# Kernel optimization log

Hardware: AMD Instinct MI355X
Metric: run time of the kernel (lower is better)

Reference implementation:

```python
import jax, jax.numpy as jnp
import numpy as np

GRID_ROWS, GRID_COLS = 7, 10
GRID_SIZE = GRID_ROWS * GRID_COLS  # 70
CONTEXT_SIZE = 24
STATE_SIZE = GRID_SIZE + CONTEXT_SIZE  # 94
H = 128  # LSTM_HIDDEN


def setup_inputs() -> dict:
    key = jax.random.key(0)
    ks = jax.random.split(key, 16)
    B, T = 1024, 128
    inp = {
        'states_seq': jax.random.normal(ks[0], (B, T, STATE_SIZE), jnp.float32),
        'actions_seq': jax.random.randint(ks[1], (B, T), 0, 4).astype(jnp.int32),
        # conv params (OIHW)
        'conv1_w': jax.random.normal(ks[2], (16, 1, 3, 3), jnp.float32) * 0.3,
        'conv1_b': jnp.zeros((16,), jnp.float32),
        'conv2_w': jax.random.normal(ks[3], (32, 16, 3, 3), jnp.float32) * 0.08,
        'conv2_b': jnp.zeros((32,), jnp.float32),
        # dense params (out, in) like torch Linear
        'grid_fc_w': jax.random.normal(ks[4], (128, 32 * GRID_SIZE), jnp.float32) * 0.02,
        'grid_fc_b': jnp.zeros((128,), jnp.float32),
        'ctx_fc_w': jax.random.normal(ks[5], (64, CONTEXT_SIZE), jnp.float32) * 0.2,
        'ctx_fc_b': jnp.zeros((64,), jnp.float32),
        'trunk_w': jax.random.normal(ks[6], (128, 192), jnp.float32) * 0.07,
        'trunk_b': jnp.zeros((128,), jnp.float32),
        # LSTM params
        'W_ih': jax.random.normal(ks[7], (4 * H, 128), jnp.float32) * 0.09,
        'b_ih': jnp.zeros((4 * H,), jnp.float32),
        'W_hh': jax.random.normal(ks[8], (4 * H, H), jnp.float32) * 0.09,
        # heads
        'actor_w': jax.random.uniform(ks[9], (4, H), jnp.float32, -0.01, 0.01),
        'actor_b': jnp.zeros((4,), jnp.float32),
        'critic_w': jax.random.uniform(ks[10], (1, H), jnp.float32, -0.01, 0.01),
        'critic_b': jnp.zeros((1,), jnp.float32),
    }
    return inp


def _forward(states_seq, actions_seq, conv1_w, conv1_b, conv2_w, conv2_b,
             grid_fc_w, grid_fc_b, ctx_fc_w, ctx_fc_b, trunk_w, trunk_b,
             W_ih, b_ih, W_hh, actor_w, actor_b, critic_w, critic_b):
    B, T, _ = states_seq.shape
    x = states_seq.reshape(-1, STATE_SIZE)                  # (N, 94)
    grid = x[:, :GRID_SIZE].reshape(-1, 1, GRID_ROWS, GRID_COLS)
    ctx = x[:, GRID_SIZE:]
    g = jax.lax.conv_general_dilated(grid, conv1_w, (1, 1), 'SAME',
                                     dimension_numbers=('NCHW', 'OIHW', 'NCHW'))
    g = jax.nn.relu(g + conv1_b[None, :, None, None])
    g = jax.lax.conv_general_dilated(g, conv2_w, (1, 1), 'SAME',
                                     dimension_numbers=('NCHW', 'OIHW', 'NCHW'))
    g = jax.nn.relu(g + conv2_b[None, :, None, None])
    g = g.reshape(g.shape[0], -1)                           # (N, 2240)
    g = jax.nn.relu(g @ grid_fc_w.T + grid_fc_b)            # (N, 128)
    c = jax.nn.relu(ctx @ ctx_fc_w.T + ctx_fc_b)            # (N, 64)
    trunk = jax.nn.relu(jnp.concatenate([g, c], -1) @ trunk_w.T + trunk_b)
    trunk = trunk.reshape(B, T, 128)

    # LSTM: precompute input-to-gate GEMM for all timesteps, scan over time
    gates_x = jnp.einsum('btd,gd->tbg', trunk, W_ih) + b_ih  # (T, B, 4H)

    def step(carry, gx):
        h, cst = carry
        gates = gx + h @ W_hh.T
        i, f, gg, o = jnp.split(gates, 4, axis=-1)
        i, f, o = jax.nn.sigmoid(i), jax.nn.sigmoid(f), jax.nn.sigmoid(o)
        gg = jnp.tanh(gg)
        cst = f * cst + i * gg
        h = o * jnp.tanh(cst)
        return (h, cst), h

    h0 = jnp.zeros((B, H), trunk.dtype)
    _, hs = jax.lax.scan(step, (h0, h0), gates_x)            # hs: (T, B, H)
    h_flat = jnp.transpose(hs, (1, 0, 2)).reshape(B * T, H)

    logits = h_flat @ actor_w.T + actor_b                    # (N, 4)
    values = (h_flat @ critic_w.T + critic_b)[:, 0]          # (N,)
    logp = jax.nn.log_softmax(logits, axis=-1)
    a = actions_seq.reshape(-1)
    log_probs = jnp.take_along_axis(logp, a[:, None].astype(jnp.int32), axis=-1)[:, 0]
    entropy = -jnp.sum(jnp.exp(logp) * logp, axis=-1)
    return log_probs, values, entropy


def reference(states_seq, actions_seq, conv1_w, conv1_b, conv2_w, conv2_b,
              grid_fc_w, grid_fc_b, ctx_fc_w, ctx_fc_b, trunk_w, trunk_b,
              W_ih, b_ih, W_hh, actor_w, actor_b, critic_w, critic_b):
    return _forward(states_seq, actions_seq, conv1_w, conv1_b, conv2_w, conv2_b,
                    grid_fc_w, grid_fc_b, ctx_fc_w, ctx_fc_b, trunk_w, trunk_b,
                    W_ih, b_ih, W_hh, actor_w, actor_b, critic_w, critic_b)
```

## Files before the change

### kernel.cpp

```cpp
#include <hip/hip_runtime.h>
#include <hip/hip_bf16.h>

typedef unsigned int  u32;
typedef unsigned short u16;
typedef unsigned long long u64;
typedef __attribute__((ext_vector_type(8))) short bf16x8;
typedef __attribute__((ext_vector_type(4))) float f32x4;

#define B_   1024
#define T_   128
#define NBT  (B_*T_)
#define CHUNK 32768
#define NCHUNK 4

#define WG_OFF   0
#define WT_OFF   286720
#define WIH_OFF  311296
#define W2_OFF   376832
#define W1C_OFF  381952
#define CVT_TOTAL 382464

#define TRUNK_OFF (1ull<<20)
#define H_OFF     (36ull<<20)
#define CTX_OFF   (72ull<<20)
#define C2_OFF    (92ull<<20)

__device__ __forceinline__ u16 f2bf(float f){
  __hip_bfloat16 h = __float2bfloat16(f);
  return *reinterpret_cast<u16*>(&h);
}
__device__ __forceinline__ float bf2f(u16 u){ return __uint_as_float((u32)u << 16); }
__device__ __forceinline__ float sigm(float x){ return 1.f / (1.f + __expf(-x)); }
__device__ __forceinline__ float tanh_f(float x){ return 2.f / (1.f + __expf(-2.f*x)) - 1.f; }

__device__ __forceinline__ void bar_lds() {
  __builtin_amdgcn_sched_barrier(0);
  asm volatile("s_waitcnt lgkmcnt(0)" ::: "memory");
  __builtin_amdgcn_s_barrier();
  __builtin_amdgcn_sched_barrier(0);
}

__global__ void k_cvt(const float* __restrict__ gfw, const float* __restrict__ tw,
                      const float* __restrict__ wih, const float* __restrict__ c2w,
                      const float* __restrict__ c1w, u16* __restrict__ wsb) {
  int i = blockIdx.x * 256 + threadIdx.x;
  if (i >= CVT_TOTAL) return;
  float v;
  if (i < WT_OFF) {
    int o = i / 2240; int k = i - o*2240;
    int pos = k >> 5, ch = k & 31;
    v = gfw[o*2240 + ch*70 + pos];
  }
  else if (i < WIH_OFF)  v = tw[i - WT_OFF];
  else if (i < W2_OFF)   v = wih[i - WIH_OFF];
  else if (i < W1C_OFF) {
    int j = i - W2_OFF; int co = j / 160; int k = j - co*160;
    int tap = k >> 4; int ci = k & 15;
    v = (tap < 9) ? c2w[co*144 + ci*9 + tap] : 0.f;
  } else {
    int j = i - W1C_OFF; int ch = j >> 5; int k = j & 31;
    v = (k < 9) ? c1w[ch*9 + k] : 0.f;
  }
  wsb[i] = f2bf(v);
}

__global__ __launch_bounds__(512, 4) void k_conv(
    const float* __restrict__ states,
    const float* __restrict__ c1b, const float* __restrict__ c2b,
    const float* __restrict__ cfw, const float* __restrict__ cfb,
    const u16* __restrict__ wsb,
    u16* __restrict__ c2g,
    u16* __restrict__ ctxg)
{
  __shared__ float s_st[8][96];
  __shared__ __align__(16) u16 act1[8*108*16];

  const int tid  = threadIdx.x;
  const int lane = tid & 63;
  const int w    = tid >> 6;
  const int arow = lane & 15;
  const int grp  = lane >> 4;
  const int g0   = blockIdx.x * 64;

  bf16x8 Bc1 = *(const bf16x8*)(wsb + W1C_OFF + arow*32 + grp*8);
  bf16x8 b2f[5][2];
  #pragma unroll
  for (int p = 0; p < 5; p++)
    #pragma unroll
    for (int nt = 0; nt < 2; nt++)
      b2f[p][nt] = *(const bf16x8*)(wsb + W2_OFF + (nt*16 + arow)*160 + p*32 + grp*8);
  float c1bv[4], c2bv0[4], c2bv1[4];
  #pragma unroll
  for (int r = 0; r < 4; r++) {
    c1bv[r]  = c1b[grp*4 + r];
    c2bv0[r] = c2b[grp*4 + r];
    c2bv1[r] = c2b[16 + grp*4 + r];
  }
  const float cfbr = cfb[lane];
  float cfwr[24];
  #pragma unroll
  for (int k = 0; k < 24; k++) cfwr[k] = cfw[lane*24 + k];

  const int sst_s = (tid*2)/94, sst_c = (tid*2)%94;

  if (tid < 376) {
    float2 v = *(const float2*)(states + (size_t)g0*94 + tid*2);
    *(float2*)&s_st[sst_s][sst_c] = v;
  }
  for (int i = tid; i < 608; i += 512) {
    int s = i / 76; int r = i - s*76; int hi2 = r >> 1; int h = r & 1;
    int hp;
    if (hi2 < 12)      hp = hi2;
    else if (hi2 < 24) hp = 96 + (hi2 - 12);
    else if (hi2 < 31) hp = (hi2 - 23) * 12;
    else               hp = (hi2 - 30) * 12 + 11;
    u32 a = (u32)((s*108 + hp)*32 + h*16) ^ (u32)((hp & 7) << 4);
    *(uint4*)((char*)act1 + a) = (uint4){0,0,0,0};
  }
  bar_lds();

  const bf16x8 zv = {0,0,0,0,0,0,0,0};

  for (int g = 0; g < 8; g++) {
    const int m0 = g0 + g*8;
    float2 npre;
    const bool haspre = (g < 7) && (tid < 376);
    if (haspre)
      npre = *(const float2*)(states + (size_t)(m0 + 8)*94 + tid*2);

    for (int mt = w; mt < 35; mt += 8) {
      int row = mt*16 + arow;
      int s = (int)(((u32)row * 59919u) >> 22); int pos = row - s*70;
      int y = (int)(((u32)pos * 6554u) >> 16);  int x = pos - y*10;
      bf16x8 pf = zv;
      if (grp == 0) {
        const float* gs = &s_st[s][0];
        #pragma unroll
        for (int t = 0; t < 8; t++) {
          int dy = t/3, dx = t - (t/3)*3;
          int yy = y + dy - 1, xx = x + dx - 1;
          bool ok = (yy >= 0) & (yy < 7) & (xx >= 0) & (xx < 10);
          float v = gs[ok ? yy*10 + xx : 0];
          pf[t] = (short)f2bf(ok ? v : 0.f);
        }
      } else if (grp == 1) {
        int yy = y + 1, xx = x + 1;
        bool ok = (yy < 7) & (xx < 10);
        float v = s_st[s][ok ? yy*10 + xx : 0];
        pf[0] = (short)f2bf(ok ? v : 0.f);
      }
      f32x4 acc = __builtin_amdgcn_mfma_f32_16x16x32_bf16(Bc1, pf, (f32x4){0.f,0.f,0.f,0.f}, 0, 0, 0);
      int hp = (y+1)*12 + (x+1);
      u16 q0 = f2bf(fmaxf(acc[0] + c1bv[0], 0.f));
      u16 q1 = f2bf(fmaxf(acc[1] + c1bv[1], 0.f));
      u16 q2 = f2bf(fmaxf(acc[2] + c1bv[2], 0.f));
      u16 q3 = f2bf(fmaxf(acc[3] + c1bv[3], 0.f));
      u64 pk = (u64)q0 | ((u64)q1 << 16) | ((u64)q2 << 32) | ((u64)q3 << 48);
      u32 wa = (u32)(((s*108 + hp)*16 + grp*4)*2) ^ (u32)((hp & 7) << 4);
      *(u64*)((char*)act1 + wa) = pk;
    }
    bar_lds();

    for (int mt = w; mt < 35; mt += 8) {
      int row = mt*16 + arow;
      int s = (int)(((u32)row * 59919u) >> 22); int pos = row - s*70;
      int y = (int)(((u32)pos * 6554u) >> 16);  int x = pos - y*10;
      f32x4 acc0 = {0.f,0.f,0.f,0.f}, acc1 = {0.f,0.f,0.f,0.f};
      #pragma unroll
      for (int p = 0; p < 5; p++) {
        int tap = p*2 + (grp >> 1); if (tap > 8) tap = 8;
        int dy = (tap * 11) >> 5; int dx = tap - dy*3;
        int hp = (y + dy)*12 + (x + dx);
        u32 ra = (u32)(((s*108 + hp)*16 + (grp & 1)*8)*2) ^ (u32)((hp & 7) << 4);
        bf16x8 bv = *(const bf16x8*)((const char*)act1 + ra);
        acc0 = __builtin_amdgcn_mfma_f32_16x16x32_bf16(b2f[p][0], bv, acc0, 0, 0, 0);
        acc1 = __builtin_amdgcn_mfma_f32_16x16x32_bf16(b2f[p][1], bv, acc1, 0, 0, 0);
      }
      {
        u16 q0 = f2bf(fmaxf(acc0[0] + c2bv0[0], 0.f));
        u16 q1 = f2bf(fmaxf(acc0[1] + c2bv0[1], 0.f));
        u16 q2 = f2bf(fmaxf(acc0[2] + c2bv0[2], 0.f));
        u16 q3 = f2bf(fmaxf(acc0[3] + c2bv0[3], 0.f));
        u64 pk = (u64)q0 | ((u64)q1 << 16) | ((u64)q2 << 32) | ((u64)q3 << 48);
        *(u64*)(c2g + (size_t)(m0 + s)*2240 + pos*32 + grp*4) = pk;
      }
      {
        u16 q0 = f2bf(fmaxf(acc1[0] + c2bv1[0], 0.f));
        u16 q1 = f2bf(fmaxf(acc1[1] + c2bv1[1], 0.f));
        u16 q2 = f2bf(fmaxf(acc1[2] + c2bv1[2], 0.f));
        u16 q3 = f2bf(fmaxf(acc1[3] + c2bv1[3], 0.f));
        u64 pk = (u64)q0 | ((u64)q1 << 16) | ((u64)q2 << 32) | ((u64)q3 << 48);
        *(u64*)(c2g + (size_t)(m0 + s)*2240 + pos*32 + 16 + grp*4) = pk;
      }
    }
    {
      float a = cfbr;
      #pragma unroll
      for (int k = 0; k < 24; k++) a = fmaf(cfwr[k], s_st[w][70 + k], a);
      ctxg[(size_t)(m0 + w)*64 + lane] = f2bf(fmaxf(a, 0.f));
    }

    if (g < 7) {
      bar_lds();
      if (haspre) *(float2*)&s_st[sst_s][sst_c] = npre;
      bar_lds();
    }
  }
}

__global__ __launch_bounds__(512, 2) void k_gemm(
    const u16* __restrict__ c2g, const u16* __restrict__ ctxg,
    const float* __restrict__ gfb, const float* __restrict__ tbv,
    const u16* __restrict__ wsb, u16* __restrict__ trunk_ws, int nbase)
{
  __shared__ __align__(16) u16 s_b[2][128*72];
  __shared__ __align__(16) u16 s_g[64*204];

  const int tid  = threadIdx.x;
  const int lane = tid & 63;
  const int w    = tid >> 6;
  const int arow = lane & 15;
  const int grp  = lane >> 4;
  const int wm   = w & 3;
  const int wn   = w >> 2;
  const int m0   = blockIdx.x * 64;

  float gfbv[4], tbvv[4];
  #pragma unroll
  for (int q = 0; q < 4; q++) {
    gfbv[q] = gfb[(wn*4 + q)*16 + arow];
    tbvv[q] = tbv[(wn*4 + q)*16 + arow];
  }

  const int srow = tid >> 2, sseg = (tid & 3) * 16;
  const u16* wg = wsb + WG_OFF;
  const u16* ap = c2g + (size_t)(m0 + wm*16 + arow) * 2240 + grp*8;

  {
    const u16* src = wg + (size_t)srow*2240 + sseg;
    *(uint4*)&s_b[0][srow*72 + sseg]     = *(const uint4*)src;
    *(uint4*)&s_b[0][srow*72 + sseg + 8] = *(const uint4*)(src + 8);
  }
  bf16x8 aC0 = *(const bf16x8*)(ap);
  bf16x8 aC1 = *(const bf16x8*)(ap + 32);
  bf16x8 aN0 = *(const bf16x8*)(ap + 64);
  bf16x8 aN1 = *(const bf16x8*)(ap + 96);
  f32x4 acc[4];
  #pragma unroll
  for (int q = 0; q < 4; q++) acc[q] = (f32x4){0.f,0.f,0.f,0.f};
  __syncthreads();

  for (int kp = 0; kp < 35; kp++) {
    uint4 b0v, b1v;
    if (kp < 34) {
      const u16* src = wg + (size_t)srow*2240 + (kp+1)*64 + sseg;
      b0v = *(const uint4*)src;
      b1v = *(const uint4*)(src + 8);
    }
    bf16x8 aF0 = aN0, aF1 = aN1;
    if (kp < 33) {
      aF0 = *(const bf16x8*)(ap + (size_t)(kp+2)*64);
      aF1 = *(const bf16x8*)(ap + (size_t)(kp+2)*64 + 32);
    }
    const u16* sb = &s_b[kp & 1][0];
    #pragma unroll
    for (int q = 0; q < 4; q++) {
      bf16x8 bv0 = *(const bf16x8*)&sb[((wn*4 + q)*16 + arow)*72 + grp*8];
      acc[q] = __builtin_amdgcn_mfma_f32_16x16x32_bf16(aC0, bv0, acc[q], 0, 0, 0);
    }
    #pragma unroll
    for (int q = 0; q < 4; q++) {
      bf16x8 bv1 = *(const bf16x8*)&sb[((wn*4 + q)*16 + arow)*72 + 32 + grp*8];
      acc[q] = __builtin_amdgcn_mfma_f32_16x16x32_bf16(aC1, bv1, acc[q], 0, 0, 0);
    }
    if (kp < 34) {
      *(uint4*)&s_b[(kp+1) & 1][srow*72 + sseg]     = b0v;
      *(uint4*)&s_b[(kp+1) & 1][srow*72 + sseg + 8] = b1v;
    }
    aC0 = aN0; aC1 = aN1; aN0 = aF0; aN1 = aF1;
    bar_lds();
  }

  #pragma unroll
  for (int q = 0; q < 4; q++)
    #pragma unroll
    for (int r = 0; r < 4; r++)
      s_g[(wm*16 + grp*4 + r)*204 + (wn*4 + q)*16 + arow] = f2bf(fmaxf(acc[q][r] + gfbv[q], 0.f));
  {
    int row = tid >> 3, seg = (tid & 7) * 8;
    uint4 c0 = *(const uint4*)(ctxg + (size_t)(m0 + row)*64 + seg);
    *(uint4*)&s_g[row*204 + 128 + seg] = c0;
  }
  bar_lds();

  f32x4 tacc[4];
  #pragma unroll
  for (int q = 0; q < 4; q++) tacc[q] = (f32x4){0.f,0.f,0.f,0.f};
  #pragma unroll
  for (int ks = 0; ks < 6; ks++) {
    bf16x8 av = *(const bf16x8*)&s_g[(wm*16 + arow)*204 + ks*32 + grp*8];
    #pragma unroll
    for (int q = 0; q < 4; q++) {
      bf16x8 bv = *(const bf16x8*)(wsb + WT_OFF + (size_t)((wn*4 + q)*16 + arow)*192 + ks*32 + grp*8);
      tacc[q] = __builtin_amdgcn_mfma_f32_16x16x32_bf16(av, bv, tacc[q], 0, 0, 0);
    }
  }
  bar_lds();
  #pragma unroll
  for (int q = 0; q < 4; q++)
    #pragma unroll
    for (int r = 0; r < 4; r++)
      s_g[(wm*16 + grp*4 + r)*204 + (wn*4 + q)*16 + arow] = f2bf(fmaxf(tacc[q][r] + tbvv[q], 0.f));
  bar_lds();

  {
    const int t0 = (nbase + m0) & 127;
    const int bb = (nbase + m0) >> 7;
    int row = tid >> 3, seg = (tid & 7) * 16;
    #pragma unroll
    for (int j = 0; j < 2; j++) {
      uint4 v = *(const uint4*)&s_g[row*204 + seg + j*8];
      *(uint4*)(trunk_ws + ((size_t)(t0 + row)*B_ + bb)*128 + seg + j*8) = v;
    }
  }
}

__global__ __launch_bounds__(512, 1) void k_lstm(
    const u16* __restrict__ trunk_ws, const float* __restrict__ whh,
    const float* __restrict__ wih, const float* __restrict__ bih,
    u16* __restrict__ h_ws)
{
  __shared__ __align__(16) u16 s_h[2][16*136];
  __shared__ __align__(16) u16 s_tk[3][4*136];

  const int tid  = threadIdx.x;
  const int lane = tid & 63;
  const int w    = tid >> 6;
  const int arow = lane & 15;
  const int grp  = lane >> 4;
  const int b0   = blockIdx.x * 4;

  bf16x8 Bv[4][4], Bw[4][4];
  float bihv[4];
  #pragma unroll
  for (int j = 0; j < 4; j++) {
    const int row = j*128 + w*16 + arow;
    bihv[j] = bih[row];
    #pragma unroll
    for (int ks = 0; ks < 4; ks++) {
      const float* s1 = whh + (size_t)row*128 + ks*32 + grp*8;
      const float* s2 = wih + (size_t)row*128 + ks*32 + grp*8;
      float4 a0 = *(const float4*)s1, a1 = *(const float4*)(s1 + 4);
      float4 b0v = *(const float4*)s2, b1v = *(const float4*)(s2 + 4);
      bf16x8 t1, t2;
      t1[0]=(short)f2bf(a0.x); t1[1]=(short)f2bf(a0.y); t1[2]=(short)f2bf(a0.z); t1[3]=(short)f2bf(a0.w);
      t1[4]=(short)f2bf(a1.x); t1[5]=(short)f2bf(a1.y); t1[6]=(short)f2bf(a1.z); t1[7]=(short)f2bf(a1.w);
      t2[0]=(short)f2bf(b0v.x); t2[1]=(short)f2bf(b0v.y); t2[2]=(short)f2bf(b0v.z); t2[3]=(short)f2bf(b0v.w);
      t2[4]=(short)f2bf(b1v.x); t2[5]=(short)f2bf(b1v.y); t2[6]=(short)f2bf(b1v.z); t2[7]=(short)f2bf(b1v.w);
      Bv[j][ks] = t1; Bw[j][ks] = t2;
    }
  }

  for (int i = tid; i < 2*16*136; i += 512) ((u16*)s_h)[i] = 0;

  const int prow = tid >> 4, pseg = (tid & 15) * 8;
  if (tid < 64) {
    #pragma unroll
    for (int s = 0; s < 3; s++)
      *(uint4*)&s_tk[s][prow*136 + pseg] =
          *(const uint4*)(trunk_ws + ((size_t)s*B_ + b0 + prow)*128 + pseg);
  }
  uint4 P0 = {0,0,0,0};
  if (tid < 64)
    P0 = *(const uint4*)(trunk_ws + ((size_t)3*B_ + b0 + prow)*128 + pseg);

  float cst = 0.f;
  __syncthreads();

  f32x4 xA[4];
  #pragma unroll
  for (int j = 0; j < 4; j++) xA[j] = (f32x4){0.f,0.f,0.f,0.f};
  #pragma unroll
  for (int ks = 0; ks < 4; ks++) {
    bf16x8 av = *(const bf16x8*)&s_tk[0][(arow & 3)*136 + ks*32 + grp*8];
    #pragma unroll
    for (int j = 0; j < 4; j++)
      xA[j] = __builtin_amdgcn_mfma_f32_16x16x32_bf16(av, Bw[j][ks], xA[j], 0, 0, 0);
  }

  for (int t = 0; t < T_; t++) {
    const int p = t & 1;

    uint4 P1 = {0,0,0,0};
    if ((t + 4 < T_) && tid < 64)
      P1 = *(const uint4*)(trunk_ws + ((size_t)(t+4)*B_ + b0 + prow)*128 + pseg);

    if (t > 0 && tid < 64) {
      uint4 hv = *(const uint4*)&s_h[p][prow*136 + pseg];
      *(uint4*)(h_ws + ((size_t)(t-1)*B_ + b0 + prow)*128 + pseg) = hv;
    }

    f32x4 racc[4], xB[4];
    #pragma unroll
    for (int j = 0; j < 4; j++) { racc[j] = (f32x4){0.f,0.f,0.f,0.f}; xB[j] = (f32x4){0.f,0.f,0.f,0.f}; }
    #pragma unroll
    for (int ks = 0; ks < 4; ks++) {
      bf16x8 av = *(const bf16x8*)&s_h[p][arow*136 + ks*32 + grp*8];
      #pragma unroll
      for (int j = 0; j < 4; j++)
        racc[j] = __builtin_amdgcn_mfma_f32_16x16x32_bf16(av, Bv[j][ks], racc[j], 0, 0, 0);
    }
    {
      const u16* tk = &s_tk[(t+1) % 3][0];
      #pragma unroll
      for (int ks = 0; ks < 4; ks++) {
        bf16x8 av = *(const bf16x8*)&tk[(arow & 3)*136 + ks*32 + grp*8];
        #pragma unroll
        for (int j = 0; j < 4; j++)
          xB[j] = __builtin_amdgcn_mfma_f32_16x16x32_bf16(av, Bw[j][ks], xB[j], 0, 0, 0);
      }
    }

    float g4[4];
    #pragma unroll
    for (int j = 0; j < 4; j++) {
      float s0 = racc[j][0] + xA[j][0];
      float s1 = racc[j][1] + xA[j][1];
      float s2 = racc[j][2] + xA[j][2];
      float s3 = racc[j][3] + xA[j][3];
      float t0v = __shfl(s0, arow);
      float t1v = __shfl(s1, arow);
      float t2v = __shfl(s2, arow);
      float t3v = __shfl(s3, arow);
      g4[j] = (grp == 0) ? t0v : (grp == 1) ? t1v : (grp == 2) ? t2v : t3v;
    }

    {
      float xi = g4[0] + bihv[0];
      float xf = g4[1] + bihv[1];
      float xg = g4[2] + bihv[2];
      float xo = g4[3] + bihv[3];
      float I = sigm(xi), F = sigm(xf), O = sigm(xo), G = tanh_f(xg);
      cst = F*cst + I*G;
      float hvv = O * tanh_f(cst);
      s_h[1-p][grp*136 + w*16 + arow] = f2bf(hvv);
    }

    if ((t + 3 < T_) && tid < 64)
      *(uint4*)&s_tk[t % 3][prow*136 + pseg] = P0;
    P0 = P1;
    #pragma unroll
    for (int j = 0; j < 4; j++) xA[j] = xB[j];
    bar_lds();
  }

  if (tid < 64) {
    uint4 hv = *(const uint4*)&s_h[T_ & 1][prow*136 + pseg];
    *(uint4*)(h_ws + ((size_t)(T_-1)*B_ + b0 + prow)*128 + pseg) = hv;
  }
}

__global__ __launch_bounds__(256, 1) void k_heads(
    const u16* __restrict__ h_ws, const int* __restrict__ actions,
    const float* __restrict__ aw, const float* __restrict__ ab,
    const float* __restrict__ cw, const float* __restrict__ cb,
    float* __restrict__ out)
{
  const int tid  = threadIdx.x;
  const int lane = tid & 63;
  const int w    = tid >> 6;
  const int arow = lane & 15;
  const int grp  = lane >> 4;

  bf16x8 Ah[4];
  #pragma unroll
  for (int ks = 0; ks < 4; ks++) {
    bf16x8 v = {0,0,0,0,0,0,0,0};
    if (arow < 4) {
      const float* src = aw + arow*128 + ks*32 + grp*8;
      #pragma unroll
      for (int j = 0; j < 8; j++) v[j] = (short)f2bf(src[j]);
    } else if (arow == 4) {
      const float* src = cw + ks*32 + grp*8;
      #pragma unroll
      for (int j = 0; j < 8; j++) v[j] = (short)f2bf(src[j]);
    }
    Ah[ks] = v;
  }
  const float ab0=ab[0], ab1=ab[1], ab2=ab[2], ab3=ab[3], cb0=cb[0];

  #pragma unroll
  for (int g = 0; g < 4; g++) {
    int m0 = (blockIdx.x*4 + w)*64 + g*16;
    int t  = m0 >> 10; int bb = m0 & 1023;
    f32x4 acc = {0.f,0.f,0.f,0.f};
    #pragma unroll
    for (int ks = 0; ks < 4; ks++) {
      bf16x8 bv = *(const bf16x8*)(h_ws + ((size_t)t*B_ + bb + arow)*128 + ks*32 + grp*8);
      acc = __builtin_amdgcn_mfma_f32_16x16x32_bf16(Ah[ks], bv, acc, 0, 0, 0);
    }
    float cr = __shfl_xor(acc[0], 16);
    if (grp == 0) {
      float L0 = acc[0] + ab0, L1 = acc[1] + ab1, L2 = acc[2] + ab2, L3 = acc[3] + ab3;
      float Lv = cr + cb0;
      float mm = fmaxf(fmaxf(L0, L1), fmaxf(L2, L3));
      float e0 = __expf(L0-mm), e1 = __expf(L1-mm), e2 = __expf(L2-mm), e3 = __expf(L3-mm);
      float S = e0+e1+e2+e3; float lse = __logf(S);
      float p0=L0-mm-lse, p1=L1-mm-lse, p2=L2-mm-lse, p3=L3-mm-lse;
      int n = (bb + arow)*T_ + t;
      int a = actions[n];
      float lpa = (a==0)?p0:(a==1)?p1:(a==2)?p2:p3;
      float ent = -(e0*p0 + e1*p1 + e2*p2 + e3*p3) / S;
      out[n] = lpa; out[NBT + n] = Lv; out[2*NBT + n] = ent;
    }
  }
}

extern "C" void kernel_launch(void* const* d_in, const int* in_sizes, int n_in,
                              void* d_out, int out_size, void* d_ws, size_t ws_size,
                              hipStream_t stream) {
  const float* states = (const float*)d_in[0];
  const int*   actions= (const int*)  d_in[1];
  const float* c1w = (const float*)d_in[2];
  const float* c1b = (const float*)d_in[3];
  const float* c2w = (const float*)d_in[4];
  const float* c2b = (const float*)d_in[5];
  const float* gfw = (const float*)d_in[6];
  const float* gfb = (const float*)d_in[7];
  const float* cfw = (const float*)d_in[8];
  const float* cfb = (const float*)d_in[9];
  const float* tw  = (const float*)d_in[10];
  const float* tbv = (const float*)d_in[11];
  const float* wih = (const float*)d_in[12];
  const float* bih = (const float*)d_in[13];
  const float* whh = (const float*)d_in[14];
  const float* aw  = (const float*)d_in[15];
  const float* ab  = (const float*)d_in[16];
  const float* cw  = (const float*)d_in[17];
  const float* cb  = (const float*)d_in[18];
  float* out = (float*)d_out;

  u16* wsb   = (u16*)d_ws;
  u16* trunk = (u16*)((char*)d_ws + TRUNK_OFF);
  u16* h_ws  = (u16*)((char*)d_ws + H_OFF);
  u16* ctxg  = (u16*)((char*)d_ws + CTX_OFF);
  u16* c2g   = (u16*)((char*)d_ws + C2_OFF);

  k_cvt<<<(CVT_TOTAL + 255)/256, 256, 0, stream>>>(gfw, tw, wih, c2w, c1w, wsb);

  for (int c = 0; c < NCHUNK; c++) {
    const float* st_c = states + (size_t)c * CHUNK * 94;
    u16* ctx_c = ctxg + (size_t)c * CHUNK * 64;
    k_conv<<<CHUNK/64, 512, 0, stream>>>(st_c, c1b, c2b, cfw, cfb, wsb, c2g, ctx_c);
    k_gemm<<<CHUNK/64, 512, 0, stream>>>(c2g, ctx_c, gfb, tbv, wsb, trunk, c*CHUNK);
  }
  k_lstm<<<B_/4, 512, 0, stream>>>(trunk, whh, wih, bih, h_ws);
  k_heads<<<512, 256, 0, stream>>>(h_ws, actions, aw, ab, cw, cb, out);
}
```

Baseline: 690.3 us.

## Software-pipeline conv and gemm stages in a fused kernel with double buffers

Replaces the alternating conv and gemm launches per chunk with one fused kernel per step. Each launch runs the conv of chunk i in some blocks and the gemm of chunk i-1 in the others, using two ping-pong intermediate buffers and a smaller chunk size. The aim is to overlap the compute-heavy conv with the gemm and cut per-launch tail idle time. In exchange the fused kernel uses a shared LDS footprint sized for the larger stage with launch bounds of 2, which lowers conv occupancy, and there are more launches.

```diff
diff --git a/kernel.cpp b/kernel.cpp
--- a/kernel.cpp
+++ b/kernel.cpp
@@ -10,8 +10,8 @@
 #define B_   1024
 #define T_   128
 #define NBT  (B_*T_)
-#define CHUNK 32768
-#define NCHUNK 4
+#define CH   16384
+#define NCH  8
 
 #define WG_OFF   0
 #define WT_OFF   286720
@@ -23,7 +23,8 @@
 #define TRUNK_OFF (1ull<<20)
 #define H_OFF     (36ull<<20)
 #define CTX_OFF   (72ull<<20)
-#define C2_OFF    (92ull<<20)
+#define C2A_OFF   (92ull<<20)
+#define C2B_OFF   (C2A_OFF + 74ull*1024*1024)
 
 __device__ __forceinline__ u16 f2bf(float f){
   __hip_bfloat16 h = __float2bfloat16(f);
@@ -64,23 +65,22 @@
   wsb[i] = f2bf(v);
 }
 
-__global__ __launch_bounds__(512, 4) void k_conv(
-    const float* __restrict__ states,
+__device__ void conv_body(char* smem,
+    const float* __restrict__ states_c,
     const float* __restrict__ c1b, const float* __restrict__ c2b,
     const float* __restrict__ cfw, const float* __restrict__ cfb,
     const u16* __restrict__ wsb,
-    u16* __restrict__ c2g,
-    u16* __restrict__ ctxg)
+    u16* __restrict__ c2buf, u16* __restrict__ ctx_c, int blk)
 {
-  __shared__ float s_st[8][96];
-  __shared__ __align__(16) u16 act1[8*108*16];
+  float (*s_st)[96] = (float(*)[96])smem;
+  u16* act1 = (u16*)(smem + 3072);
 
   const int tid  = threadIdx.x;
   const int lane = tid & 63;
   const int w    = tid >> 6;
   const int arow = lane & 15;
   const int grp  = lane >> 4;
-  const int g0   = blockIdx.x * 64;
+  const int g0   = blk * 64;
 
   bf16x8 Bc1 = *(const bf16x8*)(wsb + W1C_OFF + arow*32 + grp*8);
   bf16x8 b2f[5][2];
@@ -104,7 +104,7 @@
   const int sst_s = (tid*2)/94, sst_c = (tid*2)%94;
 
   if (tid < 376) {
-    float2 v = *(const float2*)(states + (size_t)g0*94 + tid*2);
+    float2 v = *(const float2*)(states_c + (size_t)g0*94 + tid*2);
     *(float2*)&s_st[sst_s][sst_c] = v;
   }
   for (int i = tid; i < 608; i += 512) {
@@ -115,7 +115,7 @@
     else if (hi2 < 31) hp = (hi2 - 23) * 12;
     else               hp = (hi2 - 30) * 12 + 11;
     u32 a = (u32)((s*108 + hp)*32 + h*16) ^ (u32)((hp & 7) << 4);
-    *(uint4*)((char*)act1 + a) = (uint4){0,0,0,0};
+    *(uint4*)(act1 ? (char*)act1 + a : 0) = (uint4){0,0,0,0};
   }
   bar_lds();
 
@@ -126,7 +126,7 @@
     float2 npre;
     const bool haspre = (g < 7) && (tid < 376);
     if (haspre)
-      npre = *(const float2*)(states + (size_t)(m0 + 8)*94 + tid*2);
+      npre = *(const float2*)(states_c + (size_t)(m0 + 8)*94 + tid*2);
 
     for (int mt = w; mt < 35; mt += 8) {
       int row = mt*16 + arow;
@@ -182,7 +182,7 @@
         u16 q2 = f2bf(fmaxf(acc0[2] + c2bv0[2], 0.f));
         u16 q3 = f2bf(fmaxf(acc0[3] + c2bv0[3], 0.f));
         u64 pk = (u64)q0 | ((u64)q1 << 16) | ((u64)q2 << 32) | ((u64)q3 << 48);
-        *(u64*)(c2g + (size_t)(m0 + s)*2240 + pos*32 + grp*4) = pk;
+        *(u64*)(c2buf + (size_t)(m0 + s)*2240 + pos*32 + grp*4) = pk;
       }
       {
         u16 q0 = f2bf(fmaxf(acc1[0] + c2bv1[0], 0.f));
@@ -190,14 +190,14 @@
         u16 q2 = f2bf(fmaxf(acc1[2] + c2bv1[2], 0.f));
         u16 q3 = f2bf(fmaxf(acc1[3] + c2bv1[3], 0.f));
         u64 pk = (u64)q0 | ((u64)q1 << 16) | ((u64)q2 << 32) | ((u64)q3 << 48);
-        *(u64*)(c2g + (size_t)(m0 + s)*2240 + pos*32 + 16 + grp*4) = pk;
+        *(u64*)(c2buf + (size_t)(m0 + s)*2240 + pos*32 + 16 + grp*4) = pk;
       }
     }
     {
       float a = cfbr;
       #pragma unroll
       for (int k = 0; k < 24; k++) a = fmaf(cfwr[k], s_st[w][70 + k], a);
-      ctxg[(size_t)(m0 + w)*64 + lane] = f2bf(fmaxf(a, 0.f));
+      ctx_c[(size_t)(m0 + w)*64 + lane] = f2bf(fmaxf(a, 0.f));
     }
 
     if (g < 7) {
@@ -208,13 +208,14 @@
   }
 }
 
-__global__ __launch_bounds__(512, 2) void k_gemm(
-    const u16* __restrict__ c2g, const u16* __restrict__ ctxg,
+__device__ void gemm_body(char* smem,
+    const u16* __restrict__ c2buf, const u16* __restrict__ ctx_c,
     const float* __restrict__ gfb, const float* __restrict__ tbv,
-    const u16* __restrict__ wsb, u16* __restrict__ trunk_ws, int nbase)
+    const u16* __restrict__ wsb, u16* __restrict__ trunk_ws,
+    int nbase, int blk)
 {
-  __shared__ __align__(16) u16 s_b[2][128*72];
-  __shared__ __align__(16) u16 s_g[64*204];
+  u16* s_b = (u16*)smem;
+  u16* s_g = (u16*)(smem + 36864);
 
   const int tid  = threadIdx.x;
   const int lane = tid & 63;
@@ -223,7 +224,7 @@
   const int grp  = lane >> 4;
   const int wm   = w & 3;
   const int wn   = w >> 2;
-  const int m0   = blockIdx.x * 64;
+  const int m0   = blk * 64;
 
   float gfbv[4], tbvv[4];
   #pragma unroll
@@ -234,12 +235,12 @@
 
   const int srow = tid >> 2, sseg = (tid & 3) * 16;
   const u16* wg = wsb + WG_OFF;
-  const u16* ap = c2g + (size_t)(m0 + wm*16 + arow) * 2240 + grp*8;
+  const u16* ap = c2buf + (size_t)(m0 + wm*16 + arow) * 2240 + grp*8;
 
   {
     const u16* src = wg + (size_t)srow*2240 + sseg;
-    *(uint4*)&s_b[0][srow*72 + sseg]     = *(const uint4*)src;
-    *(uint4*)&s_b[0][srow*72 + sseg + 8] = *(const uint4*)(src + 8);
+    *(uint4*)&s_b[srow*72 + sseg]     = *(const uint4*)src;
+    *(uint4*)&s_b[srow*72 + sseg + 8] = *(const uint4*)(src + 8);
   }
   bf16x8 aC0 = *(const bf16x8*)(ap);
   bf16x8 aC1 = *(const bf16x8*)(ap + 32);
@@ -262,7 +263,7 @@
       aF0 = *(const bf16x8*)(ap + (size_t)(kp+2)*64);
       aF1 = *(const bf16x8*)(ap + (size_t)(kp+2)*64 + 32);
     }
-    const u16* sb = &s_b[kp & 1][0];
+    const u16* sb = &s_b[(kp & 1)*9216];
     #pragma unroll
     for (int q = 0; q < 4; q++) {
       bf16x8 bv0 = *(const bf16x8*)&sb[((wn*4 + q)*16 + arow)*72 + grp*8];
@@ -274,8 +275,8 @@
       acc[q] = __builtin_amdgcn_mfma_f32_16x16x32_bf16(aC1, bv1, acc[q], 0, 0, 0);
     }
     if (kp < 34) {
-      *(uint4*)&s_b[(kp+1) & 1][srow*72 + sseg]     = b0v;
-      *(uint4*)&s_b[(kp+1) & 1][srow*72 + sseg + 8] = b1v;
+      *(uint4*)&s_b[((kp+1) & 1)*9216 + srow*72 + sseg]     = b0v;
+      *(uint4*)&s_b[((kp+1) & 1)*9216 + srow*72 + sseg + 8] = b1v;
     }
     aC0 = aN0; aC1 = aN1; aN0 = aF0; aN1 = aF1;
     bar_lds();
@@ -288,7 +289,7 @@
       s_g[(wm*16 + grp*4 + r)*204 + (wn*4 + q)*16 + arow] = f2bf(fmaxf(acc[q][r] + gfbv[q], 0.f));
   {
     int row = tid >> 3, seg = (tid & 7) * 8;
-    uint4 c0 = *(const uint4*)(ctxg + (size_t)(m0 + row)*64 + seg);
+    uint4 c0 = *(const uint4*)(ctx_c + (size_t)(m0 + row)*64 + seg);
     *(uint4*)&s_g[row*204 + 128 + seg] = c0;
   }
   bar_lds();
@@ -322,6 +323,30 @@
       uint4 v = *(const uint4*)&s_g[row*204 + seg + j*8];
       *(uint4*)(trunk_ws + ((size_t)(t0 + row)*B_ + bb)*128 + seg + j*8) = v;
     }
+  }
+}
+
+__global__ __launch_bounds__(512, 2) void k_fused(
+    const float* __restrict__ states,
+    const float* __restrict__ c1b, const float* __restrict__ c2b,
+    const float* __restrict__ cfw, const float* __restrict__ cfb,
+    const float* __restrict__ gfb, const float* __restrict__ tbv,
+    const u16* __restrict__ wsb,
+    u16* __restrict__ c2a, u16* __restrict__ c2bb,
+    u16* __restrict__ ctxg, u16* __restrict__ trunk_ws,
+    int i, int nconv)
+{
+  __shared__ __align__(16) char smem[62976];
+  if ((int)blockIdx.x < nconv) {
+    const float* st_c = states + (size_t)i * CH * 94;
+    u16* c2w_  = (i & 1) ? c2bb : c2a;
+    u16* ctx_c = ctxg + (size_t)i * CH * 64;
+    conv_body(smem, st_c, c1b, c2b, cfw, cfb, wsb, c2w_, ctx_c, blockIdx.x);
+  } else {
+    const int c = i - 1;
+    const u16* c2r   = (c & 1) ? c2bb : c2a;
+    const u16* ctx_c = ctxg + (size_t)c * CH * 64;
+    gemm_body(smem, c2r, ctx_c, gfb, tbv, wsb, trunk_ws, c*CH, blockIdx.x - nconv);
   }
 }
 
@@ -544,15 +569,17 @@
   u16* trunk = (u16*)((char*)d_ws + TRUNK_OFF);
   u16* h_ws  = (u16*)((char*)d_ws + H_OFF);
   u16* ctxg  = (u16*)((char*)d_ws + CTX_OFF);
-  u16* c2g   = (u16*)((char*)d_ws + C2_OFF);
+  u16* c2a   = (u16*)((char*)d_ws + C2A_OFF);
+  u16* c2bb  = (u16*)((char*)d_ws + C2B_OFF);
 
   k_cvt<<<(CVT_TOTAL + 255)/256, 256, 0, stream>>>(gfw, tw, wih, c2w, c1w, wsb);
 
-  for (int c = 0; c < NCHUNK; c++) {
-    const float* st_c = states + (size_t)c * CHUNK * 94;
-    u16* ctx_c = ctxg + (size_t)c * CHUNK * 64;
-    k_conv<<<CHUNK/64, 512, 0, stream>>>(st_c, c1b, c2b, cfw, cfb, wsb, c2g, ctx_c);
-    k_gemm<<<CHUNK/64, 512, 0, stream>>>(c2g, ctx_c, gfb, tbv, wsb, trunk, c*CHUNK);
+  for (int i = 0; i <= NCH; i++) {
+    const int nconv = (i < NCH) ? (CH/64) : 0;
+    const int ngemm = (i > 0)   ? (CH/64) : 0;
+    k_fused<<<nconv + ngemm, 512, 0, stream>>>(states, c1b, c2b, cfw, cfb,
+                                               gfb, tbv, wsb, c2a, c2bb,
+                                               ctxg, trunk, i, nconv);
   }
   k_lstm<<<B_/4, 512, 0, stream>>>(trunk, whh, wih, bih, h_ws);
   k_heads<<<512, 256, 0, stream>>>(h_ws, actions, aw, ab, cw, cb, out);
```

Result: slower. 784.7 us (+13.7%).
